# Kernel tuning notes

Measured on AMD Instinct MI355X. Metric: run time of the kernel, lower is better.

Reference implementation:

```python
import jax, jax.numpy as jnp
import numpy as np

B, S, D, H = 2, 2048, 1024, 16
HD = D // H  # head_dim = 64

def setup_inputs() -> dict:
    key = jax.random.key(0)
    ks = jax.random.split(key, 12)
    sc = 0.02
    return {
        "x": jax.random.normal(ks[0], (B, S, D), dtype=jnp.float32),
        "docking_scores": jax.random.uniform(ks[1], (B, S), dtype=jnp.float32),
        # weights stored as (in, out): y = x @ W + b (equivalent to torch Linear with W=weight.T)
        "Wq": jax.random.normal(ks[2], (D, D), dtype=jnp.float32) * sc,
        "bq": jnp.zeros((D,), dtype=jnp.float32),
        "Wk": jax.random.normal(ks[3], (D, D), dtype=jnp.float32) * sc,
        "bk": jnp.zeros((D,), dtype=jnp.float32),
        "Wv": jax.random.normal(ks[4], (D, D), dtype=jnp.float32) * sc,
        "bv": jnp.zeros((D,), dtype=jnp.float32),
        "Wo": jax.random.normal(ks[5], (D, D), dtype=jnp.float32) * sc,
        "bo": jnp.zeros((D,), dtype=jnp.float32),
        "beta": jnp.asarray(0.5, dtype=jnp.float32),
    }

def reference(x, docking_scores, Wq, bq, Wk, bk, Wv, bv, Wo, bo, beta):
    b, s, d = x.shape
    # project and split heads: (B, H, S, HD)
    def heads(y):
        return y.reshape(b, s, H, HD).transpose(0, 2, 1, 3)
    Q = heads(x @ Wq + bq)
    K = heads(x @ Wk + bk)
    V = heads(x @ Wv + bv)
    # full attention scores (B, H, S, S) — materialized as in the source
    scores = jnp.einsum('bhqd,bhkd->bhqk', Q, K) / np.float32(np.sqrt(HD))
    attn = jax.nn.softmax(scores, axis=-1)
    # docking blend: daa_type != ALL -> blend with per-key docking scores
    ds = docking_scores[:, None, None, :]  # (B, 1, 1, S)
    attn = (1.0 - beta) * attn + beta * ds
    ctx = jnp.einsum('bhqk,bhkd->bhqd', attn, V)
    ctx = ctx.transpose(0, 2, 1, 3).reshape(b, s, d)
    return ctx @ Wo + bo
```

## Files before the change

### kernel.cpp

```cpp
#include <hip/hip_runtime.h>

typedef __attribute__((ext_vector_type(8))) short short8;
typedef __attribute__((ext_vector_type(4))) short short4v;
typedef __attribute__((ext_vector_type(4))) float f32x4;

#if __has_builtin(__builtin_amdgcn_exp2f)
#define EXP2F(x) __builtin_amdgcn_exp2f(x)
#define QSCALE 0.1803368801111601f
#else
#define EXP2F(x) __expf(x)
#define QSCALE 0.125f
#endif

__device__ __forceinline__ short f2bf(float f) {
  unsigned u = __builtin_bit_cast(unsigned, f);
  u += 0x7fffu + ((u >> 16) & 1u);
  return (short)(u >> 16);
}
__device__ __forceinline__ float bf2f(short s) {
  unsigned u = ((unsigned)(unsigned short)s) << 16;
  return __builtin_bit_cast(float, u);
}
__device__ __forceinline__ void async_load16(const short* g, short* l) {
  __builtin_amdgcn_global_load_lds(
      (const __attribute__((address_space(1))) unsigned int*)g,
      (__attribute__((address_space(3))) unsigned int*)l, 16, 0, 0);
}

__global__ __launch_bounds__(256) void fused_pre(
    const float* __restrict__ x, short* __restrict__ xb,
    const float* __restrict__ W0, const float* __restrict__ W1,
    const float* __restrict__ W2, const float* __restrict__ W3,
    short* __restrict__ T0, short* __restrict__ T1,
    short* __restrict__ T2, short* __restrict__ T3) {
  __shared__ float tile[32][33];
  if (blockIdx.x < 4096) {
    int i = (blockIdx.x * 256 + threadIdx.x) * 4;
    float4 v = *(const float4*)(x + i);
    short4v o;
    o[0] = f2bf(v.x); o[1] = f2bf(v.y); o[2] = f2bf(v.z); o[3] = f2bf(v.w);
    *(short4v*)(xb + i) = o;
    return;
  }
  int bid = blockIdx.x - 4096;
  int z = bid >> 10;
  int by = (bid >> 5) & 31, bx = bid & 31;
  const float* W; short* T;
  switch (z) {
    case 0: W = W0; T = T0; break;
    case 1: W = W1; T = T1; break;
    case 2: W = W2; T = T2; break;
    default: W = W3; T = T3; break;
  }
  int tx = threadIdx.x & 31, ty = threadIdx.x >> 5;
  int c = bx * 32 + tx;
  #pragma unroll
  for (int i = 0; i < 4; ++i) {
    int r = by * 32 + ty + i * 8;
    tile[ty + i * 8][tx] = W[(size_t)r * 1024 + c];
  }
  __syncthreads();
  int k = by * 32 + tx;
  #pragma unroll
  for (int i = 0; i < 4; ++i) {
    int n = bx * 32 + ty + i * 8;
    T[(size_t)n * 1024 + k] = f2bf(tile[tx][ty + i * 8]);
  }
}

__device__ __forceinline__ void gemm_core_128_bk64(
    const short* __restrict__ A, const short* __restrict__ Bt,
    int m0, int n0, short* As, short* Bs, f32x4 acc[4][4]) {
  const int tid = threadIdx.x;
  const int wave = tid >> 6, lane = tid & 63;
  const int wm = wave >> 1, wn = wave & 1;
  const int lr = lane & 15, quad = lane >> 4;
  const int l7 = lr & 7;
  const int r8 = lane >> 3, cb = lane & 7;
  const int src = (cb ^ r8) << 3;
  for (int k0 = 0; k0 < 1024; k0 += 64) {
    __syncthreads();
    #pragma unroll
    for (int jj = 0; jj < 4; ++jj) {
      int j = wave * 4 + jj;
      int row = j * 8 + r8;
      async_load16(A + (size_t)(m0 + row) * 1024 + k0 + src, As + j * 512 + lane * 8);
      async_load16(Bt + (size_t)(n0 + row) * 1024 + k0 + src, Bs + j * 512 + lane * 8);
    }
    __syncthreads();
    #pragma unroll
    for (int c = 0; c < 2; ++c) {
      short8 af[4], bfr[4];
      #pragma unroll
      for (int i = 0; i < 4; ++i) {
        int ra = wm * 64 + i * 16 + lr;
        af[i] = *(const short8*)(As + ra * 64 + ((((c * 4 + quad) ^ l7)) << 3));
        int rb = wn * 64 + i * 16 + lr;
        bfr[i] = *(const short8*)(Bs + rb * 64 + ((((c * 4 + quad) ^ l7)) << 3));
      }
      #pragma unroll
      for (int i = 0; i < 4; ++i)
        #pragma unroll
        for (int j = 0; j < 4; ++j)
          acc[i][j] = __builtin_amdgcn_mfma_f32_16x16x32_bf16(af[i], bfr[j], acc[i][j], 0, 0, 0);
    }
  }
}

__global__ __launch_bounds__(256, 2) void qkv_gemm(
    const short* __restrict__ xb,
    const short* __restrict__ WqT, const short* __restrict__ WkT, const short* __restrict__ WvT,
    const float* __restrict__ bq, const float* __restrict__ bk, const float* __restrict__ bv,
    short* __restrict__ Qb, short* __restrict__ Kb, short* __restrict__ Vt) {
  __shared__ short As[128 * 64];
  __shared__ short Bs[128 * 64];
  int which = blockIdx.x >> 3;
  int n0 = (blockIdx.x & 7) * 128;
  int m0 = blockIdx.y * 128;
  const short* Bt = (which == 0) ? WqT : (which == 1) ? WkT : WvT;
  const float* bias = (which == 0) ? bq : (which == 1) ? bk : bv;
  f32x4 acc[4][4] = {};
  gemm_core_128_bk64(xb, Bt, m0, n0, As, Bs, acc);
  const int lane = threadIdx.x & 63, wave = threadIdx.x >> 6;
  const int wm = wave >> 1, wn = wave & 1;
  const int lr = lane & 15, quad = lane >> 4;
  if (which < 2) {
    short* Out = (which == 0) ? Qb : Kb;
    const float scale = (which == 0) ? QSCALE : 1.0f;
    #pragma unroll
    for (int i = 0; i < 4; ++i)
      #pragma unroll
      for (int j = 0; j < 4; ++j) {
        int col = n0 + wn * 64 + j * 16 + lr;
        float bb = bias[col];
        int rowb = m0 + wm * 64 + i * 16 + quad * 4;
        #pragma unroll
        for (int r = 0; r < 4; ++r)
          Out[(size_t)(rowb + r) * 1024 + col] = f2bf((acc[i][j][r] + bb) * scale);
      }
  } else {
    #pragma unroll
    for (int i = 0; i < 4; ++i)
      #pragma unroll
      for (int j = 0; j < 4; ++j) {
        int col = n0 + wn * 64 + j * 16 + lr;
        float bb = bias[col];
        int h = col >> 6, d = col & 63;
        int rowb = m0 + wm * 64 + i * 16 + quad * 4;
        int b = rowb >> 11, s = rowb & 2047;
        short4v pk;
        #pragma unroll
        for (int r = 0; r < 4; ++r) pk[r] = f2bf(acc[i][j][r] + bb);
        *(short4v*)(Vt + ((size_t)(b * 16 + h) * 64 + d) * 2048 + s) = pk;
      }
  }
}

__global__ __launch_bounds__(256) void dsv_kernel(const short* __restrict__ Vt,
                                                  const float* __restrict__ ds,
                                                  float* __restrict__ dsV) {
  int bh = blockIdx.x;
  int b = bh >> 4;
  int tid = threadIdx.x;
  int d = tid >> 2, part = tid & 3;
  const short* vrow = Vt + ((size_t)bh * 64 + d) * 2048 + part * 512;
  const float* dsrow = ds + (size_t)b * 2048 + part * 512;
  float acc = 0.f;
  for (int i = 0; i < 512; i += 8) {
    short8 v = *(const short8*)(vrow + i);
    float4 f0 = *(const float4*)(dsrow + i);
    float4 f1 = *(const float4*)(dsrow + i + 4);
    acc += f0.x * bf2f(v[0]) + f0.y * bf2f(v[1]) + f0.z * bf2f(v[2]) + f0.w * bf2f(v[3]);
    acc += f1.x * bf2f(v[4]) + f1.y * bf2f(v[5]) + f1.z * bf2f(v[6]) + f1.w * bf2f(v[7]);
  }
  acc += __shfl_xor(acc, 1);
  acc += __shfl_xor(acc, 2);
  if (part == 0) dsV[bh * 64 + d] = acc;
}

__global__ __launch_bounds__(256, 2) void attn_kernel(
    const short* __restrict__ Qb, const short* __restrict__ Kb,
    const short* __restrict__ Vt, const float* __restrict__ dsV,
    const float* __restrict__ beta_p, short* __restrict__ ctx) {
  __shared__ short smem[32768];
  const int tid = threadIdx.x, wave = tid >> 6, lane = tid & 63;
  const int bh = blockIdx.x >> 4, qt = blockIdx.x & 15;
  const int b = bh >> 4, h = bh & 15;
  const size_t bS = (size_t)b * 2048;
  const int lr = lane & 15, quad = lane >> 4;
  const int qg = wave & 1, half = wave >> 1;
  const int q0 = qt * 128 + qg * 64;
  const int l7 = lr & 7;

  short* Ksh = smem + half * 8192;
  short* Vsh = Ksh + 4096;
  short* myP = smem + 16384 + wave * 4096;

  short8 qf[4][2];
  #pragma unroll
  for (int mb = 0; mb < 4; ++mb)
    #pragma unroll
    for (int c = 0; c < 2; ++c)
      qf[mb][c] = *(const short8*)(Qb + (bS + q0 + mb * 16 + lr) * 1024 + h * 64 + c * 32 + quad * 8);

  f32x4 O[4][4] = {};
  float lacc[4] = {0.f, 0.f, 0.f, 0.f};

  const int srow = lane >> 3;
  const int scb = (lane & 7) ^ srow;

  for (int t = 0; t < 16; ++t) {
    const int k0 = (half * 16 + t) * 64;
    __syncthreads();
    if (qg == 0) {
      #pragma unroll
      for (int c = 0; c < 8; ++c) {
        int rk = c * 8 + srow;
        async_load16(Kb + (bS + k0 + rk) * 1024 + h * 64 + scb * 8, Ksh + c * 512);
      }
    } else {
      #pragma unroll
      for (int c = 0; c < 8; ++c) {
        int rv = c * 8 + srow;
        async_load16(Vt + ((size_t)bh * 64 + rv) * 2048 + k0 + scb * 8, Vsh + c * 512);
      }
    }
    __syncthreads();

    #pragma unroll
    for (int kb = 0; kb < 4; ++kb) {
      const short* kr = Ksh + (kb * 16 + lr) * 64;
      short8 kf0 = *(const short8*)(kr + ((quad ^ l7) << 3));
      short8 kf1 = *(const short8*)(kr + (((4 + quad) ^ l7) << 3));
      #pragma unroll
      for (int mb = 0; mb < 4; ++mb) {
        f32x4 st = {0.f, 0.f, 0.f, 0.f};
        st = __builtin_amdgcn_mfma_f32_16x16x32_bf16(kf0, qf[mb][0], st, 0, 0, 0);
        st = __builtin_amdgcn_mfma_f32_16x16x32_bf16(kf1, qf[mb][1], st, 0, 0, 0);
        float p0 = EXP2F(st[0]), p1 = EXP2F(st[1]);
        float p2 = EXP2F(st[2]), p3 = EXP2F(st[3]);
        lacc[mb] += (p0 + p1) + (p2 + p3);
        unsigned a0 = __builtin_bit_cast(unsigned, p0) + 0x8000u;
        unsigned a1 = __builtin_bit_cast(unsigned, p1) + 0x8000u;
        unsigned a2 = __builtin_bit_cast(unsigned, p2) + 0x8000u;
        unsigned a3 = __builtin_bit_cast(unsigned, p3) + 0x8000u;
        uint2 pk;
        pk.x = __builtin_amdgcn_perm(a1, a0, 0x07060302u);
        pk.y = __builtin_amdgcn_perm(a3, a2, 0x07060302u);
        int phys = (4 * kb + quad) ^ (2 * l7);
        *(uint2*)(myP + (mb * 16 + lr) * 64 + phys * 4) = pk;
      }
    }
    #pragma unroll
    for (int kc = 0; kc < 2; ++kc) {
      short8 pf[4];
      #pragma unroll
      for (int mb = 0; mb < 4; ++mb) {
        int phys = (8 * kc + 2 * quad) ^ (2 * l7);
        pf[mb] = *(const short8*)(myP + (mb * 16 + lr) * 64 + phys * 4);
      }
      #pragma unroll
      for (int db = 0; db < 4; ++db) {
        const short* vr = Vsh + (db * 16 + lr) * 64;
        short8 vf = *(const short8*)(vr + (((kc * 4 + quad) ^ l7) << 3));
        #pragma unroll
        for (int mb = 0; mb < 4; ++mb)
          O[mb][db] = __builtin_amdgcn_mfma_f32_16x16x32_bf16(vf, pf[mb], O[mb][db], 0, 0, 0);
      }
    }
  }

  float* Obuf = (float*)smem;
  float* lbuf = (float*)(smem + 16384);
  const int qs = (quad + lr) & 3;
  __syncthreads();
  if (half == 1) {
    #pragma unroll
    for (int mb = 0; mb < 4; ++mb) {
      #pragma unroll
      for (int db = 0; db < 4; ++db)
        *(f32x4*)(Obuf + ((qg * 4 + mb) * 4 + db) * 256 + lr * 16 + qs * 4) = O[mb][db];
      lbuf[(qg * 4 + mb) * 64 + quad * 16 + lr] = lacc[mb];
    }
  }
  __syncthreads();
  if (half == 0) {
    float beta = *beta_p;
    #pragma unroll
    for (int mb = 0; mb < 4; ++mb) {
      #pragma unroll
      for (int db = 0; db < 4; ++db)
        O[mb][db] += *(const f32x4*)(Obuf + ((qg * 4 + mb) * 4 + db) * 256 + lr * 16 + qs * 4);
      float v = lacc[mb] + lbuf[(qg * 4 + mb) * 64 + quad * 16 + lr];
      v += __shfl_xor(v, 16);
      v += __shfl_xor(v, 32);
      float linv = (1.f - beta) / v;
      #pragma unroll
      for (int db = 0; db < 4; ++db) {
        float4 dv = *(const float4*)(dsV + bh * 64 + db * 16 + quad * 4);
        short4v o;
        o[0] = f2bf(O[mb][db][0] * linv + beta * dv.x);
        o[1] = f2bf(O[mb][db][1] * linv + beta * dv.y);
        o[2] = f2bf(O[mb][db][2] * linv + beta * dv.z);
        o[3] = f2bf(O[mb][db][3] * linv + beta * dv.w);
        *(short4v*)(ctx + (bS + q0 + mb * 16 + lr) * 1024 + h * 64 + db * 16 + quad * 4) = o;
      }
    }
  }
}

__global__ __launch_bounds__(256, 2) void out_gemm(
    const short* __restrict__ ctx, const short* __restrict__ WoT,
    const float* __restrict__ bo, float* __restrict__ out) {
  __shared__ short As[64 * 64];
  __shared__ short Bs[128 * 64];
  const int n0 = blockIdx.x * 128, m0 = blockIdx.y * 64;
  const int tid = threadIdx.x, wave = tid >> 6, lane = tid & 63;
  const int wm = wave >> 1, wn = wave & 1;
  const int lr = lane & 15, quad = lane >> 4;
  const int l7 = lr & 7;
  const int r8 = lane >> 3, cb = lane & 7;
  const int src = (cb ^ r8) << 3;
  f32x4 acc[2][4] = {};
  for (int k0 = 0; k0 < 1024; k0 += 64) {
    __syncthreads();
    #pragma unroll
    for (int jj = 0; jj < 2; ++jj) {
      int j = wave * 2 + jj;
      int row = j * 8 + r8;
      async_load16(ctx + (size_t)(m0 + row) * 1024 + k0 + src, As + j * 512 + lane * 8);
    }
    #pragma unroll
    for (int jj = 0; jj < 4; ++jj) {
      int j = wave * 4 + jj;
      int row = j * 8 + r8;
      async_load16(WoT + (size_t)(n0 + row) * 1024 + k0 + src, Bs + j * 512 + lane * 8);
    }
    __syncthreads();
    #pragma unroll
    for (int c = 0; c < 2; ++c) {
      short8 af[2], bfr[4];
      #pragma unroll
      for (int i = 0; i < 2; ++i) {
        int ra = wm * 32 + i * 16 + lr;
        af[i] = *(const short8*)(As + ra * 64 + (((c * 4 + quad) ^ l7) << 3));
      }
      #pragma unroll
      for (int j = 0; j < 4; ++j) {
        int rb = wn * 64 + j * 16 + lr;
        bfr[j] = *(const short8*)(Bs + rb * 64 + (((c * 4 + quad) ^ l7) << 3));
      }
      #pragma unroll
      for (int i = 0; i < 2; ++i)
        #pragma unroll
        for (int j = 0; j < 4; ++j)
          acc[i][j] = __builtin_amdgcn_mfma_f32_16x16x32_bf16(af[i], bfr[j], acc[i][j], 0, 0, 0);
    }
  }
  #pragma unroll
  for (int i = 0; i < 2; ++i)
    #pragma unroll
    for (int j = 0; j < 4; ++j) {
      int col = n0 + wn * 64 + j * 16 + lr;
      float bb = bo[col];
      int rowb = m0 + wm * 32 + i * 16 + quad * 4;
      #pragma unroll
      for (int r = 0; r < 4; ++r)
        out[(size_t)(rowb + r) * 1024 + col] = acc[i][j][r] + bb;
    }
}

extern "C" void kernel_launch(void* const* d_in, const int* in_sizes, int n_in,
                              void* d_out, int out_size, void* d_ws, size_t ws_size,
                              hipStream_t stream) {
  const float* x    = (const float*)d_in[0];
  const float* dsc  = (const float*)d_in[1];
  const float* Wq   = (const float*)d_in[2];
  const float* bq   = (const float*)d_in[3];
  const float* Wk   = (const float*)d_in[4];
  const float* bk   = (const float*)d_in[5];
  const float* Wv   = (const float*)d_in[6];
  const float* bv   = (const float*)d_in[7];
  const float* Wo   = (const float*)d_in[8];
  const float* bo   = (const float*)d_in[9];
  const float* beta = (const float*)d_in[10];

  char* ws = (char*)d_ws;
  const size_t MB = 1u << 20;
  short* xb  = (short*)(ws + 0 * MB);
  short* WqT = (short*)(ws + 8 * MB);
  short* WkT = (short*)(ws + 10 * MB);
  short* WvT = (short*)(ws + 12 * MB);
  short* WoT = (short*)(ws + 14 * MB);
  short* Qb  = (short*)(ws + 16 * MB);
  short* Kb  = (short*)(ws + 24 * MB);
  short* Vt  = (short*)(ws + 32 * MB);
  float* dsV = (float*)(ws + 40 * MB);
  short* ctx = xb;

  fused_pre<<<8192, 256, 0, stream>>>(x, xb, Wq, Wk, Wv, Wo, WqT, WkT, WvT, WoT);
  qkv_gemm<<<dim3(24, 32), 256, 0, stream>>>(xb, WqT, WkT, WvT, bq, bk, bv, Qb, Kb, Vt);
  dsv_kernel<<<32, 256, 0, stream>>>(Vt, dsc, dsV);
  attn_kernel<<<512, 256, 0, stream>>>(Qb, Kb, Vt, dsV, beta, ctx);
  out_gemm<<<dim3(8, 64), 256, 0, stream>>>(ctx, WoT, bo, (float*)d_out);
}
```

Before: 214.9 us.

## Double-buffer K/V tiles in attention, split dsV reduction across blocks, raise qkv occupancy

The attention kernel now double-buffers its K/V shared-memory tiles, issuing async loads for the next tile before computing the current one, so there is one barrier per iteration instead of two and load latency overlaps with MFMA work. The P staging buffer is halved by interleaving the QK/softmax and PV steps per 32-key chunk, which frees LDS for the second buffer. The dsV reduction is spread over 8x more blocks using atomicAdd into a buffer zeroed by an extra block in the preprocessing kernel. qkv_gemm's launch bounds now ask for 3 blocks per CU, which may force register spilling.

```diff
diff --git a/kernel.cpp b/kernel.cpp
--- a/kernel.cpp
+++ b/kernel.cpp
@@ -32,7 +32,8 @@
     const float* __restrict__ W0, const float* __restrict__ W1,
     const float* __restrict__ W2, const float* __restrict__ W3,
     short* __restrict__ T0, short* __restrict__ T1,
-    short* __restrict__ T2, short* __restrict__ T3) {
+    short* __restrict__ T2, short* __restrict__ T3,
+    float* __restrict__ dsV) {
   __shared__ float tile[32][33];
   if (blockIdx.x < 4096) {
     int i = (blockIdx.x * 256 + threadIdx.x) * 4;
@@ -40,6 +41,12 @@
     short4v o;
     o[0] = f2bf(v.x); o[1] = f2bf(v.y); o[2] = f2bf(v.z); o[3] = f2bf(v.w);
     *(short4v*)(xb + i) = o;
+    return;
+  }
+  if (blockIdx.x == 8192) {
+    float4 z = {0.f, 0.f, 0.f, 0.f};
+    ((float4*)dsV)[threadIdx.x * 2] = z;
+    ((float4*)dsV)[threadIdx.x * 2 + 1] = z;
     return;
   }
   int bid = blockIdx.x - 4096;
@@ -107,7 +114,7 @@
   }
 }
 
-__global__ __launch_bounds__(256, 2) void qkv_gemm(
+__global__ __launch_bounds__(256, 3) void qkv_gemm(
     const short* __restrict__ xb,
     const short* __restrict__ WqT, const short* __restrict__ WkT, const short* __restrict__ WvT,
     const float* __restrict__ bq, const float* __restrict__ bk, const float* __restrict__ bv,
@@ -159,14 +166,14 @@
 __global__ __launch_bounds__(256) void dsv_kernel(const short* __restrict__ Vt,
                                                   const float* __restrict__ ds,
                                                   float* __restrict__ dsV) {
-  int bh = blockIdx.x;
+  int bh = blockIdx.x, sc = blockIdx.y;
   int b = bh >> 4;
-  int tid = threadIdx.x;
-  int d = tid >> 2, part = tid & 3;
-  const short* vrow = Vt + ((size_t)bh * 64 + d) * 2048 + part * 512;
-  const float* dsrow = ds + (size_t)b * 2048 + part * 512;
+  int d = threadIdx.x >> 2, part = threadIdx.x & 3;
+  const short* vrow = Vt + ((size_t)bh * 64 + d) * 2048 + sc * 256 + part * 64;
+  const float* dsrow = ds + (size_t)b * 2048 + sc * 256 + part * 64;
   float acc = 0.f;
-  for (int i = 0; i < 512; i += 8) {
+  #pragma unroll
+  for (int i = 0; i < 64; i += 8) {
     short8 v = *(const short8*)(vrow + i);
     float4 f0 = *(const float4*)(dsrow + i);
     float4 f1 = *(const float4*)(dsrow + i + 4);
@@ -175,14 +182,14 @@
   }
   acc += __shfl_xor(acc, 1);
   acc += __shfl_xor(acc, 2);
-  if (part == 0) dsV[bh * 64 + d] = acc;
+  if (part == 0) atomicAdd(dsV + bh * 64 + d, acc);
 }
 
 __global__ __launch_bounds__(256, 2) void attn_kernel(
     const short* __restrict__ Qb, const short* __restrict__ Kb,
     const short* __restrict__ Vt, const float* __restrict__ dsV,
     const float* __restrict__ beta_p, short* __restrict__ ctx) {
-  __shared__ short smem[32768];
+  __shared__ short smem[40960];
   const int tid = threadIdx.x, wave = tid >> 6, lane = tid & 63;
   const int bh = blockIdx.x >> 4, qt = blockIdx.x & 15;
   const int b = bh >> 4, h = bh & 15;
@@ -191,10 +198,12 @@
   const int qg = wave & 1, half = wave >> 1;
   const int q0 = qt * 128 + qg * 64;
   const int l7 = lr & 7;
-
-  short* Ksh = smem + half * 8192;
-  short* Vsh = Ksh + 4096;
-  short* myP = smem + 16384 + wave * 4096;
+  const int swz = 2 * (lr & 3);
+
+  short* myP = smem + 32768 + wave * 2048;
+
+  const int srow = lane >> 3;
+  const int scb = (lane & 7) ^ srow;
 
   short8 qf[4][2];
   #pragma unroll
@@ -206,58 +215,72 @@
   f32x4 O[4][4] = {};
   float lacc[4] = {0.f, 0.f, 0.f, 0.f};
 
-  const int srow = lane >> 3;
-  const int scb = (lane & 7) ^ srow;
+  {
+    const int k0 = (half * 16) * 64;
+    short* Ksh = smem + half * 8192;
+    short* Vsh = Ksh + 4096;
+    if (qg == 0) {
+      #pragma unroll
+      for (int c = 0; c < 8; ++c)
+        async_load16(Kb + (bS + k0 + c * 8 + srow) * 1024 + h * 64 + scb * 8, Ksh + c * 512);
+    } else {
+      #pragma unroll
+      for (int c = 0; c < 8; ++c)
+        async_load16(Vt + ((size_t)bh * 64 + c * 8 + srow) * 2048 + k0 + scb * 8, Vsh + c * 512);
+    }
+  }
+  __syncthreads();
 
   for (int t = 0; t < 16; ++t) {
-    const int k0 = (half * 16 + t) * 64;
-    __syncthreads();
-    if (qg == 0) {
-      #pragma unroll
-      for (int c = 0; c < 8; ++c) {
-        int rk = c * 8 + srow;
-        async_load16(Kb + (bS + k0 + rk) * 1024 + h * 64 + scb * 8, Ksh + c * 512);
-      }
-    } else {
-      #pragma unroll
-      for (int c = 0; c < 8; ++c) {
-        int rv = c * 8 + srow;
-        async_load16(Vt + ((size_t)bh * 64 + rv) * 2048 + k0 + scb * 8, Vsh + c * 512);
-      }
-    }
-    __syncthreads();
-
-    #pragma unroll
-    for (int kb = 0; kb < 4; ++kb) {
-      const short* kr = Ksh + (kb * 16 + lr) * 64;
-      short8 kf0 = *(const short8*)(kr + ((quad ^ l7) << 3));
-      short8 kf1 = *(const short8*)(kr + (((4 + quad) ^ l7) << 3));
+    const int cur = t & 1;
+    short* Ksh = smem + cur * 16384 + half * 8192;
+    short* Vsh = Ksh + 4096;
+    if (t < 15) {
+      const int k0n = (half * 16 + t + 1) * 64;
+      short* Kn = smem + (cur ^ 1) * 16384 + half * 8192;
+      short* Vn = Kn + 4096;
+      if (qg == 0) {
+        #pragma unroll
+        for (int c = 0; c < 8; ++c)
+          async_load16(Kb + (bS + k0n + c * 8 + srow) * 1024 + h * 64 + scb * 8, Kn + c * 512);
+      } else {
+        #pragma unroll
+        for (int c = 0; c < 8; ++c)
+          async_load16(Vt + ((size_t)bh * 64 + c * 8 + srow) * 2048 + k0n + scb * 8, Vn + c * 512);
+      }
+    }
+    #pragma unroll
+    for (int kc = 0; kc < 2; ++kc) {
+      #pragma unroll
+      for (int kbl = 0; kbl < 2; ++kbl) {
+        int kb = kc * 2 + kbl;
+        const short* kr = Ksh + (kb * 16 + lr) * 64;
+        short8 kf0 = *(const short8*)(kr + ((quad ^ l7) << 3));
+        short8 kf1 = *(const short8*)(kr + (((4 + quad) ^ l7) << 3));
+        #pragma unroll
+        for (int mb = 0; mb < 4; ++mb) {
+          f32x4 st = {0.f, 0.f, 0.f, 0.f};
+          st = __builtin_amdgcn_mfma_f32_16x16x32_bf16(kf0, qf[mb][0], st, 0, 0, 0);
+          st = __builtin_amdgcn_mfma_f32_16x16x32_bf16(kf1, qf[mb][1], st, 0, 0, 0);
+          float p0 = EXP2F(st[0]), p1 = EXP2F(st[1]);
+          float p2 = EXP2F(st[2]), p3 = EXP2F(st[3]);
+          lacc[mb] += (p0 + p1) + (p2 + p3);
+          unsigned a0 = __builtin_bit_cast(unsigned, p0) + 0x8000u;
+          unsigned a1 = __builtin_bit_cast(unsigned, p1) + 0x8000u;
+          unsigned a2 = __builtin_bit_cast(unsigned, p2) + 0x8000u;
+          unsigned a3 = __builtin_bit_cast(unsigned, p3) + 0x8000u;
+          uint2 pk;
+          pk.x = __builtin_amdgcn_perm(a1, a0, 0x07060302u);
+          pk.y = __builtin_amdgcn_perm(a3, a2, 0x07060302u);
+          int phys = (4 * kbl + quad) ^ swz;
+          *(uint2*)(myP + (mb * 16 + lr) * 32 + phys * 4) = pk;
+        }
+      }
+      short8 pf[4];
       #pragma unroll
       for (int mb = 0; mb < 4; ++mb) {
-        f32x4 st = {0.f, 0.f, 0.f, 0.f};
-        st = __builtin_amdgcn_mfma_f32_16x16x32_bf16(kf0, qf[mb][0], st, 0, 0, 0);
-        st = __builtin_amdgcn_mfma_f32_16x16x32_bf16(kf1, qf[mb][1], st, 0, 0, 0);
-        float p0 = EXP2F(st[0]), p1 = EXP2F(st[1]);
-        float p2 = EXP2F(st[2]), p3 = EXP2F(st[3]);
-        lacc[mb] += (p0 + p1) + (p2 + p3);
-        unsigned a0 = __builtin_bit_cast(unsigned, p0) + 0x8000u;
-        unsigned a1 = __builtin_bit_cast(unsigned, p1) + 0x8000u;
-        unsigned a2 = __builtin_bit_cast(unsigned, p2) + 0x8000u;
-        unsigned a3 = __builtin_bit_cast(unsigned, p3) + 0x8000u;
-        uint2 pk;
-        pk.x = __builtin_amdgcn_perm(a1, a0, 0x07060302u);
-        pk.y = __builtin_amdgcn_perm(a3, a2, 0x07060302u);
-        int phys = (4 * kb + quad) ^ (2 * l7);
-        *(uint2*)(myP + (mb * 16 + lr) * 64 + phys * 4) = pk;
-      }
-    }
-    #pragma unroll
-    for (int kc = 0; kc < 2; ++kc) {
-      short8 pf[4];
-      #pragma unroll
-      for (int mb = 0; mb < 4; ++mb) {
-        int phys = (8 * kc + 2 * quad) ^ (2 * l7);
-        pf[mb] = *(const short8*)(myP + (mb * 16 + lr) * 64 + phys * 4);
+        int phys = (2 * quad) ^ swz;
+        pf[mb] = *(const short8*)(myP + (mb * 16 + lr) * 32 + phys * 4);
       }
       #pragma unroll
       for (int db = 0; db < 4; ++db) {
@@ -268,12 +291,12 @@
           O[mb][db] = __builtin_amdgcn_mfma_f32_16x16x32_bf16(vf, pf[mb], O[mb][db], 0, 0, 0);
       }
     }
+    __syncthreads();
   }
 
   float* Obuf = (float*)smem;
-  float* lbuf = (float*)(smem + 16384);
+  float* lbuf = (float*)(smem + 32768);
   const int qs = (quad + lr) & 3;
-  __syncthreads();
   if (half == 1) {
     #pragma unroll
     for (int mb = 0; mb < 4; ++mb) {
@@ -398,9 +421,9 @@
   float* dsV = (float*)(ws + 40 * MB);
   short* ctx = xb;
 
-  fused_pre<<<8192, 256, 0, stream>>>(x, xb, Wq, Wk, Wv, Wo, WqT, WkT, WvT, WoT);
+  fused_pre<<<8193, 256, 0, stream>>>(x, xb, Wq, Wk, Wv, Wo, WqT, WkT, WvT, WoT, dsV);
   qkv_gemm<<<dim3(24, 32), 256, 0, stream>>>(xb, WqT, WkT, WvT, bq, bk, bv, Qb, Kb, Vt);
-  dsv_kernel<<<32, 256, 0, stream>>>(Vt, dsc, dsV);
+  dsv_kernel<<<dim3(32, 8), 256, 0, stream>>>(Vt, dsc, dsV);
   attn_kernel<<<512, 256, 0, stream>>>(Qb, Kb, Vt, dsV, beta, ctx);
   out_gemm<<<dim3(8, 64), 256, 0, stream>>>(ctx, WoT, bo, (float*)d_out);
 }
```

Result: faster. 201.3 us (-6.3%).
